# Kernel optimization log

Measured on AMD Instinct MI355X. Metric: run time of the kernel, lower is better.

Reference implementation:

```python
import jax, jax.numpy as jnp
import numpy as np

PAD = 1  # padding from init_kwargs

def setup_inputs() -> dict:
    key = jax.random.key(0)
    k1, k2 = jax.random.split(key)
    x = jax.random.normal(k1, (1, 256, 224, 224), dtype=jnp.float32)
    # Conv2d_mvm weight: [out_channels, in_channels, kh, kw]
    weight = jax.random.normal(k2, (256, 256, 3, 3), dtype=jnp.float32) * 0.05
    return {"x": x, "weight": weight}

def reference(x, weight):
    # Exact math of the bit-sliced crossbar conv forward: stride-1 cross-correlation
    # with zero padding, no bias, output squeezed to [C_out, H_out, W_out]
    # (the original forward emits no batch dimension).
    out = jax.lax.conv_general_dilated(
        x, weight,
        window_strides=(1, 1),
        padding=((PAD, PAD), (PAD, PAD)),
        dimension_numbers=("NCHW", "OIHW", "NCHW"),
    )
    return out[0]  # [C_out, H_out, W_out]
```

## Files before the change

### kernel.cpp

```cpp
#include <hip/hip_runtime.h>


#define H 224
#define W 224
#define NPOS (H*W)
#define CI 256
#define CO 256
#define KDIM 2304
#define HP 226
#define XP_ELEMS (HP*HP*CI)
#define AP_ELEMS (CO*KDIM)
#define BN 224

typedef __bf16 bf16x8 __attribute__((ext_vector_type(8)));
typedef float f32x4 __attribute__((ext_vector_type(4)));
typedef unsigned short u16x4 __attribute__((ext_vector_type(4)));
typedef unsigned short u16x8 __attribute__((ext_vector_type(8)));

__device__ __forceinline__ unsigned short f2bf(float f) {
    unsigned int u = __float_as_uint(f);
    u += 0x7fff + ((u >> 16) & 1);
    return (unsigned short)(u >> 16);
}

__device__ __forceinline__ void load_lds16(const unsigned short* g, unsigned short* l) {
    __builtin_amdgcn_global_load_lds(
        (const __attribute__((address_space(1))) void*)g,
        (__attribute__((address_space(3))) void*)l,
        16, 0, 0);
}

#define XT_BLOCKS 3136
#define WT_BLOCKS 256
#define BORDER_V8 28800
#define ROW_V8 7232
__global__ void prep_kernel(const float* __restrict__ x, const float* __restrict__ w,
                            unsigned short* __restrict__ ap, unsigned short* __restrict__ xp) {
    __shared__ unsigned short smem[64 * 68];
    const int bx = blockIdx.x;
    const int t = threadIdx.x;

    if (bx < XT_BLOCKS) {
        const unsigned int pBase = (unsigned int)(bx % 784) * 64;
        const unsigned int ciBase = (unsigned int)(bx / 784) * 64;
        {
            const int p4 = (t & 15) * 4;
            const int c0 = t >> 4;
#pragma unroll
            for (int i = 0; i < 4; ++i) {
                const int ci_l = c0 + i * 16;
                const f32x4 v = *(const f32x4*)&x[(ciBase + ci_l) * NPOS + pBase + p4];
                u16x4 s;
                s[0] = f2bf(v[0]); s[1] = f2bf(v[1]); s[2] = f2bf(v[2]); s[3] = f2bf(v[3]);
                *(u16x4*)&smem[ci_l * 68 + p4] = s;
            }
        }
        __syncthreads();
        {
            const int ci0 = (t & 7) * 8;
            const int pr = t >> 3;
#pragma unroll
            for (int j = 0; j < 2; ++j) {
                const int p_l = pr + j * 32;
                const unsigned int p = pBase + p_l;
                const unsigned int hi = p / W, wi = p - hi * W;
                u16x8 v;
#pragma unroll
                for (int k = 0; k < 8; ++k) v[k] = smem[(ci0 + k) * 68 + p_l];
                *(u16x8*)&xp[((hi + 1) * HP + (wi + 1)) * CI + ciBase + ci0] = v;
            }
        }
    } else if (bx < XT_BLOCKS + WT_BLOCKS) {
        const int co = bx - XT_BLOCKS;
        const float* wc = w + co * KDIM;
#pragma unroll
        for (int i = 0; i < 9; ++i)
            smem[i * 256 + t] = f2bf(wc[i * 256 + t]);
        __syncthreads();
        unsigned short* apc = ap + co * KDIM;
#pragma unroll
        for (int tap = 0; tap < 9; ++tap)
            apc[tap * 256 + t] = smem[t * 9 + tap];
    } else {
        const int idx = (bx - XT_BLOCKS - WT_BLOCKS) * 256 + t;
        if (idx < BORDER_V8) {
            unsigned short* p;
            if (idx < 2 * ROW_V8) {
                const int r = idx / ROW_V8;
                const int off = idx - r * ROW_V8;
                p = xp + r * (225 * HP * CI) + off * 8;
            } else {
                const int i2 = idx - 2 * ROW_V8;
                const int seg = i2 >> 5;
                const int o = i2 & 31;
                const int hp = 1 + (seg >> 1);
                const int wp = (seg & 1) * 225;
                p = xp + (hp * HP + wp) * CI + o * 8;
            }
            *(u16x8*)p = (u16x8){0, 0, 0, 0, 0, 0, 0, 0};
        }
    }
}


#define MFMA14(miA, miB)                                                        \
    __builtin_amdgcn_s_setprio(1);                                              \
    _Pragma("unroll")                                                           \
    for (int ni = 0; ni < 7; ++ni) {                                            \
        acc[miA][ni] = __builtin_amdgcn_mfma_f32_16x16x32_bf16(                 \
            af[miA], bf[ni], acc[miA][ni], 0, 0, 0);                            \
        acc[miB][ni] = __builtin_amdgcn_mfma_f32_16x16x32_bf16(                 \
            af[miB], bf[ni], acc[miB][ni], 0, 0, 0);                            \
    }                                                                           \
    __builtin_amdgcn_s_setprio(0);

__global__ __launch_bounds__(512, 1) void gemm_conv_kernel(
    const unsigned short* __restrict__ Ap,
    const unsigned short* __restrict__ Xp,
    float* __restrict__ out)
{
    __shared__ unsigned short lds[65536];

    const int tid = threadIdx.x;
    const int Nb = blockIdx.x;
    const int wave = tid >> 6;
    const int wm = wave >> 1;
    const int wn = wave & 1;
    const int lane = tid & 63;
    const int ln15 = lane & 15;
    const int quad = lane >> 4;
    const int slot8 = (quad ^ ((ln15 >> 1) & 3)) * 8;
    const int arow = (wm * 64 + ln15) * 32 + slot8;
    const int brow = 32768 + (wn * 112 + ln15) * 32 + slot8;

    const int c4 = (tid & 3) ^ ((tid >> 3) & 3);
    const unsigned short* a_src[2];
    const unsigned short* b_src[2];
#pragma unroll
    for (int j = 0; j < 2; ++j) {
        const int r = j * 128 + (tid >> 2);
        a_src[j] = Ap + r * KDIM + c4 * 8;
        unsigned int p = Nb * BN + r;
        unsigned int hi = p / W, wi = p - hi * W;
        b_src[j] = Xp + (hi * HP + wi) * CI + c4 * 8;
    }

    f32x4 acc[4][7];
#pragma unroll
    for (int mi = 0; mi < 4; ++mi)
#pragma unroll
        for (int ni = 0; ni < 7; ++ni)
            acc[mi][ni] = (f32x4){0.f, 0.f, 0.f, 0.f};

    auto stageA = [&](int kt, int k) {
        const int dst = ((kt & 1) * 2 + k) * 8192;
        const int off = kt * 64 + k * 32;
#pragma unroll
        for (int j = 0; j < 2; ++j)
            load_lds16(a_src[j] + off, &lds[dst + (j * 8 + wave) * 512]);
    };
    auto stageB = [&](int kt, int k) {
        const int dst = 32768 + ((kt & 1) * 2 + k) * 8192;
        const int tap = kt >> 2;
        const int dh = (tap * 11) >> 5;
        const int dw = tap - dh * 3;
        const int off = (dh * HP + dw) * CI + (kt & 3) * 64 + k * 32;
#pragma unroll
        for (int j = 0; j < 2; ++j)
            load_lds16(b_src[j] + off, &lds[dst + (j * 8 + wave) * 512]);
    };

    bf16x8 af[4], bf[7];

#define RD_MAIN(base)                                                           \
    _Pragma("unroll")                                                           \
    for (int mi = 0; mi < 2; ++mi)                                              \
        af[mi] = *(const bf16x8*)&lds[(base) + arow + mi * 512];                \
    _Pragma("unroll")                                                           \
    for (int ni = 0; ni < 7; ++ni)                                              \
        bf[ni] = *(const bf16x8*)&lds[(base) + brow + ni * 512];

#define RD_TAILA(base)                                                          \
    _Pragma("unroll")                                                           \
    for (int mi = 2; mi < 4; ++mi)                                              \
        af[mi] = *(const bf16x8*)&lds[(base) + arow + mi * 512];

    stageA(0, 0); stageB(0, 0); stageA(0, 1); stageB(0, 1);
    asm volatile("s_waitcnt vmcnt(4)" ::: "memory");
    __builtin_amdgcn_s_barrier();

    for (int kt = 0; kt < 36; ++kt) {
        const int b0 = (kt & 1) * 16384;
        const int b1 = b0 + 8192;
        const bool st = kt < 35;
        RD_MAIN(b0)
        if (st) stageA(kt + 1, 0);
        MFMA14(0, 1)
        RD_TAILA(b0)
        if (st) stageB(kt + 1, 0);
        MFMA14(2, 3)
        if (st) asm volatile("s_waitcnt vmcnt(4)" ::: "memory");
        else    asm volatile("s_waitcnt vmcnt(0)" ::: "memory");
        __builtin_amdgcn_s_barrier();
        RD_MAIN(b1)
        if (st) stageA(kt + 1, 1);
        MFMA14(0, 1)
        RD_TAILA(b1)
        if (st) stageB(kt + 1, 1);
        MFMA14(2, 3)
        if (st) {
            asm volatile("s_waitcnt vmcnt(4)" ::: "memory");
            __builtin_amdgcn_s_barrier();
        }
    }

    const int pcol = Nb * BN + wn * 112 + ln15;
    const int corow = wm * 64 + quad * 4;
#pragma unroll
    for (int mi = 0; mi < 4; ++mi)
#pragma unroll
        for (int ni = 0; ni < 7; ++ni)
#pragma unroll
            for (int r = 0; r < 4; ++r)
                out[(corow + mi * 16 + r) * NPOS + pcol + ni * 16] = acc[mi][ni][r];
}

extern "C" void kernel_launch(void* const* d_in, const int* in_sizes, int n_in,
                              void* d_out, int out_size, void* d_ws, size_t ws_size,
                              hipStream_t stream) {
    const float* x = (const float*)d_in[0];
    const float* w = (const float*)d_in[1];
    float* out = (float*)d_out;

    unsigned short* xp = (unsigned short*)d_ws;
    unsigned short* ap = xp + XP_ELEMS;

    prep_kernel<<<XT_BLOCKS + WT_BLOCKS + 113, 256, 0, stream>>>(x, w, ap, xp);
    gemm_conv_kernel<<<dim3(NPOS / BN), 512, 0, stream>>>(ap, xp, out);
}
```

Before: 153.2 us.

## Split GEMM conv into 128-row M tiles with 3-stage LDS pipeline

Replaces the 512-thread block computing all 256 output channels with 256-thread blocks that each compute 128 channels, using a 2D grid so twice as many blocks are launched. The LDS footprint shrinks and the K loop now steps 32 at a time through a triple-buffered ring with loads issued two iterations ahead, so two blocks can share a CU and global-to-LDS latency is better hidden. In exchange, each B (input) tile is loaded twice, once per M block, which raises global and L2 traffic.

```diff
diff --git a/kernel.cpp b/kernel.cpp
--- a/kernel.cpp
+++ b/kernel.cpp
@@ -114,15 +114,29 @@
     }                                                                           \
     __builtin_amdgcn_s_setprio(0);
 
-__global__ __launch_bounds__(512, 1) void gemm_conv_kernel(
+#define RD_MAIN(abase, bbase)                                                   \
+    _Pragma("unroll")                                                           \
+    for (int mi = 0; mi < 2; ++mi)                                              \
+        af[mi] = *(const bf16x8*)&lds[(abase) + arow + mi * 512];               \
+    _Pragma("unroll")                                                           \
+    for (int ni = 0; ni < 7; ++ni)                                              \
+        bf[ni] = *(const bf16x8*)&lds[(bbase) + brow + ni * 512];
+
+#define RD_TAILA(abase)                                                         \
+    _Pragma("unroll")                                                           \
+    for (int mi = 2; mi < 4; ++mi)                                              \
+        af[mi] = *(const bf16x8*)&lds[(abase) + arow + mi * 512];
+
+__global__ __launch_bounds__(256, 2) void gemm_conv_kernel(
     const unsigned short* __restrict__ Ap,
     const unsigned short* __restrict__ Xp,
     float* __restrict__ out)
 {
-    __shared__ unsigned short lds[65536];
+    __shared__ unsigned short lds[36864];
 
     const int tid = threadIdx.x;
     const int Nb = blockIdx.x;
+    const int Mb = blockIdx.y;
     const int wave = tid >> 6;
     const int wm = wave >> 1;
     const int wn = wave & 1;
@@ -131,15 +145,19 @@
     const int quad = lane >> 4;
     const int slot8 = (quad ^ ((ln15 >> 1) & 3)) * 8;
     const int arow = (wm * 64 + ln15) * 32 + slot8;
-    const int brow = 32768 + (wn * 112 + ln15) * 32 + slot8;
+    const int brow = (wn * 112 + ln15) * 32 + slot8;
 
     const int c4 = (tid & 3) ^ ((tid >> 3) & 3);
     const unsigned short* a_src[2];
-    const unsigned short* b_src[2];
+    const unsigned short* b_src[4];
 #pragma unroll
     for (int j = 0; j < 2; ++j) {
-        const int r = j * 128 + (tid >> 2);
-        a_src[j] = Ap + r * KDIM + c4 * 8;
+        const int r = j * 64 + (tid >> 2);
+        a_src[j] = Ap + (Mb * 128 + r) * KDIM + c4 * 8;
+    }
+#pragma unroll
+    for (int j = 0; j < 4; ++j) {
+        const int r = j * 64 + (tid >> 2);
         unsigned int p = Nb * BN + r;
         unsigned int hi = p / W, wi = p - hi * W;
         b_src[j] = Xp + (hi * HP + wi) * CI + c4 * 8;
@@ -152,70 +170,55 @@
         for (int ni = 0; ni < 7; ++ni)
             acc[mi][ni] = (f32x4){0.f, 0.f, 0.f, 0.f};
 
-    auto stageA = [&](int kt, int k) {
-        const int dst = ((kt & 1) * 2 + k) * 8192;
-        const int off = kt * 64 + k * 32;
+    auto stageA = [&](int kt, int buf) {
+        const int dst = buf * 4096;
+        const int off = kt * 32;
 #pragma unroll
         for (int j = 0; j < 2; ++j)
-            load_lds16(a_src[j] + off, &lds[dst + (j * 8 + wave) * 512]);
+            load_lds16(a_src[j] + off, &lds[dst + (j * 4 + wave) * 512]);
     };
-    auto stageB = [&](int kt, int k) {
-        const int dst = 32768 + ((kt & 1) * 2 + k) * 8192;
-        const int tap = kt >> 2;
+    auto stageB = [&](int kt, int buf) {
+        const int dst = 12288 + buf * 8192;
+        const int tap = kt >> 3;
         const int dh = (tap * 11) >> 5;
         const int dw = tap - dh * 3;
-        const int off = (dh * HP + dw) * CI + (kt & 3) * 64 + k * 32;
-#pragma unroll
-        for (int j = 0; j < 2; ++j)
-            load_lds16(b_src[j] + off, &lds[dst + (j * 8 + wave) * 512]);
+        const int off = (dh * HP + dw) * CI + (kt & 7) * 32;
+#pragma unroll
+        for (int j = 0; j < 4; ++j)
+            load_lds16(b_src[j] + off, &lds[dst + (j * 4 + wave) * 512]);
     };
 
     bf16x8 af[4], bf[7];
 
-#define RD_MAIN(base)                                                           \
-    _Pragma("unroll")                                                           \
-    for (int mi = 0; mi < 2; ++mi)                                              \
-        af[mi] = *(const bf16x8*)&lds[(base) + arow + mi * 512];                \
-    _Pragma("unroll")                                                           \
-    for (int ni = 0; ni < 7; ++ni)                                              \
-        bf[ni] = *(const bf16x8*)&lds[(base) + brow + ni * 512];
-
-#define RD_TAILA(base)                                                          \
-    _Pragma("unroll")                                                           \
-    for (int mi = 2; mi < 4; ++mi)                                              \
-        af[mi] = *(const bf16x8*)&lds[(base) + arow + mi * 512];
-
-    stageA(0, 0); stageB(0, 0); stageA(0, 1); stageB(0, 1);
-    asm volatile("s_waitcnt vmcnt(4)" ::: "memory");
+    stageA(0, 0); stageB(0, 0);
+    stageA(1, 1); stageB(1, 1);
+    asm volatile("s_waitcnt vmcnt(6)" ::: "memory");
     __builtin_amdgcn_s_barrier();
 
-    for (int kt = 0; kt < 36; ++kt) {
-        const int b0 = (kt & 1) * 16384;
-        const int b1 = b0 + 8192;
-        const bool st = kt < 35;
-        RD_MAIN(b0)
-        if (st) stageA(kt + 1, 0);
+    int buf = 0;
+    for (int kt = 0; kt < 72; ++kt) {
+        const int sbuf = (buf == 0) ? 2 : buf - 1;
+        const int abase = buf * 4096;
+        const int bbase = 12288 + buf * 8192;
+        const bool st = kt < 70;
+        RD_MAIN(abase, bbase)
+        if (st) stageA(kt + 2, sbuf);
         MFMA14(0, 1)
-        RD_TAILA(b0)
-        if (st) stageB(kt + 1, 0);
-        MFMA14(2, 3)
-        if (st) asm volatile("s_waitcnt vmcnt(4)" ::: "memory");
-        else    asm volatile("s_waitcnt vmcnt(0)" ::: "memory");
-        __builtin_amdgcn_s_barrier();
-        RD_MAIN(b1)
-        if (st) stageA(kt + 1, 1);
-        MFMA14(0, 1)
-        RD_TAILA(b1)
-        if (st) stageB(kt + 1, 1);
+        RD_TAILA(abase)
+        if (st) stageB(kt + 2, sbuf);
         MFMA14(2, 3)
         if (st) {
-            asm volatile("s_waitcnt vmcnt(4)" ::: "memory");
+            asm volatile("s_waitcnt vmcnt(6)" ::: "memory");
             __builtin_amdgcn_s_barrier();
-        }
+        } else if (kt == 70) {
+            asm volatile("s_waitcnt vmcnt(0)" ::: "memory");
+            __builtin_amdgcn_s_barrier();
+        }
+        buf = (buf == 2) ? 0 : buf + 1;
     }
 
     const int pcol = Nb * BN + wn * 112 + ln15;
-    const int corow = wm * 64 + quad * 4;
+    const int corow = Mb * 128 + wm * 64 + quad * 4;
 #pragma unroll
     for (int mi = 0; mi < 4; ++mi)
 #pragma unroll
@@ -236,5 +239,5 @@
     unsigned short* ap = xp + XP_ELEMS;
 
     prep_kernel<<<XT_BLOCKS + WT_BLOCKS + 113, 256, 0, stream>>>(x, w, ap, xp);
-    gemm_conv_kernel<<<dim3(NPOS / BN), 512, 0, stream>>>(ap, xp, out);
-}
+    gemm_conv_kernel<<<dim3(NPOS / BN, 2), 256, 0, stream>>>(ap, xp, out);
+}
```

Result: slower. 165.3 us (+7.9%).
